# Kernel optimization log

Hardware: AMD Instinct MI355X
Metric: run time of the kernel (lower is better)

The kernel has to match this reference:

```python
import jax, jax.numpy as jnp
import numpy as np
import math

N = 131072        # number of query points
IN_DIM = 3
G = 5             # grid_level = num_sin_layers - 2
F = 8             # feature_dims per level
W = 256           # hidden width (ffenc_dims[1:])
OUT = 64          # num_outputs
BOUND = 1.0
BASE_SIGMA = 1.0
EXP_SIGMA = 2.0
SIN_W0 = 5.0      # multires - 1 = n_levels - 1


def setup_inputs() -> dict:
    key = jax.random.key(0)
    ks = jax.random.split(key, 9)
    in_pos = jax.random.uniform(ks[0], (N, IN_DIM), jnp.float32, -BOUND, BOUND)
    grid_feats = jax.random.normal(ks[1], (N, G * F), jnp.float32) * 0.01  # grid_embed_std
    ffn_A = jax.random.normal(ks[2], (G, F, W), jnp.float32)
    # SIREN-style inits (scaled normals approximating uniform SIREN init ranges)
    W0 = jax.random.normal(ks[3], (IN_DIM, W), jnp.float32) / IN_DIM
    b0 = jax.random.normal(ks[4], (W,), jnp.float32) * 0.01
    Wh = jax.random.normal(ks[5], (G, W, W), jnp.float32) * (math.sqrt(6.0 / W) / SIN_W0)
    bh = jax.random.normal(ks[6], (G, W), jnp.float32) * 0.01
    Wh_high = jax.random.normal(ks[7], (G, W, OUT), jnp.float32) * (math.sqrt(6.0 / W) / SIN_W0)
    bh_high = jax.random.normal(ks[8], (G, OUT), jnp.float32) * 0.01
    return {"in_pos": in_pos, "grid_feats": grid_feats, "ffn_A": ffn_A,
            "W0": W0, "b0": b0, "Wh": Wh, "bh": bh,
            "Wh_high": Wh_high, "bh_high": bh_high}


def reference(in_pos, grid_feats, ffn_A, W0, b0, Wh, bh, Wh_high, bh_high):
    sigmas = BASE_SIGMA * (EXP_SIGMA ** jnp.arange(G, dtype=jnp.float32))  # [G]
    embed = lambda h: jnp.sin(SIN_W0 * h)  # dim-preserving periodic embedding

    x = in_pos / BOUND                                   # [N, 3]
    # grid branch: per-level Fourier projection of hash-grid features
    gx = jnp.transpose(grid_feats.reshape(-1, G, F), (1, 0, 2))  # [G, N, F]
    ffn = ffn_A * sigmas[:, None, None]                   # [G, F, W]
    gx = jnp.sin((2.0 * math.pi) * jnp.einsum('gnf,gfw->gnw', gx, ffn))  # [G, N, W]

    # SIREN branch, layer 0
    x = embed(x @ W0 + b0)                                # [N, W]
    x_out = jnp.zeros((x.shape[0], OUT), dtype=x.dtype)
    for l in range(G):  # layers 1 .. num_sin_layers-2
        x = embed(x @ Wh[l] + bh[l])                      # [N, W]
        x = gx[l] + x                                     # grid residual
        x_out = x_out + embed(x @ Wh_high[l] + bh_high[l])
    return x_out
```

## Files before the change

### kernel.cpp

```cpp
#include <hip/hip_runtime.h>


#define TM 64
#define XSTRIDE 264
#define GSTRIDE 48
#define K5 0.79577471545947667f

typedef __attribute__((ext_vector_type(8))) _Float16 v8h;
typedef __attribute__((ext_vector_type(2))) __fp16 hw2;
typedef __attribute__((ext_vector_type(4))) float v4f;
typedef __attribute__((ext_vector_type(16))) float v16f;

#define MFMA16H(a, b, c) __builtin_amdgcn_mfma_f32_16x16x32_f16(a, b, c, 0, 0, 0)
#define MFMA32H(a, b, c) __builtin_amdgcn_mfma_f32_32x32x16_f16(a, b, c, 0, 0, 0)

__device__ __forceinline__ float sin_rev(float u) {
#if __has_builtin(__builtin_amdgcn_fractf)
    return __builtin_amdgcn_sinf(__builtin_amdgcn_fractf(u));
#else
    return __builtin_amdgcn_sinf(u - floorf(u));
#endif
}

__device__ __forceinline__ short f16s(float x) {
    _Float16 hh = (_Float16)x;
    return __builtin_bit_cast(short, hh);
}

__global__ __launch_bounds__(256) void ffb_pack(
    const float* __restrict__ Wh, const float* __restrict__ Whh,
    const float* __restrict__ ffnA,
    short* __restrict__ wh, short* __restrict__ whh, short* __restrict__ gf)
{
    int t = blockIdx.x * 256 + threadIdx.x;
    if (t < 40960) {
        int lane = t & 63, nt = (t >> 6) & 7, kb = (t >> 9) & 15, l = t >> 13;
        int n = nt * 32 + (lane & 31);
        int k0 = kb * 16 + (lane >> 5) * 8;
        short hs[8];
        #pragma unroll
        for (int jj = 0; jj < 8; jj++)
            hs[jj] = f16s(Wh[(l * 256 + k0 + jj) * 256 + n] * K5);
        *(v8h*)(wh + t * 8) = *(v8h*)hs;
    } else if (t < 51200) {
        int t2 = t - 40960;
        int lane = t2 & 63, nt = (t2 >> 6) & 3, kb = (t2 >> 8) & 7, l = t2 >> 11;
        int n = nt * 16 + (lane & 15);
        int k0 = kb * 32 + (lane >> 4) * 8;
        short hs[8];
        #pragma unroll
        for (int jj = 0; jj < 8; jj++)
            hs[jj] = f16s(Whh[(l * 256 + k0 + jj) * 64 + n] * K5);
        *(v8h*)(whh + t2 * 8) = *(v8h*)hs;
    } else if (t < 53760) {
        int t3 = t - 51200;
        int lane = t3 & 63, nt = (t3 >> 6) & 7, l = t3 >> 9;
        int n = nt * 32 + (lane & 31);
        const float sc = 0.5f * (float)(1 << l);
        short hs[8];
        #pragma unroll
        for (int jj = 0; jj < 8; jj++)
            hs[jj] = f16s(ffnA[(l * 8 + jj) * 256 + n] * sc);
        *(v8h*)(gf + t3 * 8) = *(v8h*)hs;
    }
}

__global__ __launch_bounds__(256, 3) void ffb_main(
    const float* __restrict__ pos, const float* __restrict__ gfeat,
    const float* __restrict__ W0, const float* __restrict__ b0,
    const float* __restrict__ bh, const float* __restrict__ bhh,
    const short* __restrict__ wh, const short* __restrict__ whh,
    const short* __restrict__ gf,
    float* __restrict__ out)
{
    __shared__ __align__(16) short s_x[TM * XSTRIDE];
    __shared__ __align__(16) short s_g[TM * GSTRIDE];
    __shared__ float s_pos[TM * 3];

    const int tid = threadIdx.x;
    const int row0 = blockIdx.x * TM;
    const int lane = tid & 63;
    const int w = tid >> 6;
    const int i = lane & 15;
    const int q = lane >> 4;
    const int m32 = lane & 31;
    const int h = lane >> 5;

    if (tid < TM * 3) s_pos[tid] = pos[row0 * 3 + tid];
    for (int k2 = tid; k2 < TM * 40; k2 += 256) {
        int r = k2 / 40, f = k2 % 40;
        s_g[r * GSTRIDE + f] = f16s(gfeat[row0 * 40 + k2]);
    }
    __syncthreads();

    {
        const int c = tid;
        const float w00 = W0[c], w01 = W0[256 + c], w02 = W0[512 + c], bc = b0[c];
        #pragma unroll 4
        for (int r = 0; r < TM; r++) {
            float d = s_pos[r * 3 + 0] * w00 + s_pos[r * 3 + 1] * w01
                    + s_pos[r * 3 + 2] * w02 + bc;
            s_x[r * XSTRIDE + c] = f16s(sin_rev(d * K5));
        }
    }
    __syncthreads();

    float cout[4][4];
    #pragma unroll
    for (int m = 0; m < 4; m++)
        #pragma unroll
        for (int r = 0; r < 4; r++) cout[m][r] = 0.f;

    const int a1off0 = m32 * XSTRIDE + h * 8;
    const int a1off1 = (32 + m32) * XSTRIDE + h * 8;

    for (int l = 0; l < 5; l++) {
        const float bias0 = bh[l * 256 + w * 64 + m32] * K5;
        const float bias1 = bh[l * 256 + w * 64 + 32 + m32] * K5;
        v16f C1[2][2];
        #pragma unroll
        for (int r = 0; r < 16; r++) {
            C1[0][0][r] = bias0; C1[1][0][r] = bias0;
            C1[0][1][r] = bias1; C1[1][1][r] = bias1;
        }
        v8h gb0 = *(const v8h*)(gf + ((l * 8 + w * 2 + 0) * 64 + lane) * 8);
        v8h gb1 = *(const v8h*)(gf + ((l * 8 + w * 2 + 1) * 64 + lane) * 8);

        {
            const short* bp = wh + l * 65536 + (2 * w) * 512 + lane * 8;
            v8h rb0[4], rb1[4];
            #pragma unroll
            for (int p = 0; p < 3; p++) {
                rb0[p] = *(const v8h*)(bp + p * 4096);
                rb1[p] = *(const v8h*)(bp + p * 4096 + 512);
            }
            #pragma unroll
            for (int kb = 0; kb < 16; kb++) {
                if (kb + 3 < 16) {
                    rb0[(kb + 3) & 3] = *(const v8h*)(bp + (kb + 3) * 4096);
                    rb1[(kb + 3) & 3] = *(const v8h*)(bp + (kb + 3) * 4096 + 512);
                }
                v8h a0 = *(const v8h*)&s_x[a1off0 + kb * 16];
                v8h a1 = *(const v8h*)&s_x[a1off1 + kb * 16];
                v8h bc0 = rb0[kb & 3], bc1 = rb1[kb & 3];
                C1[0][0] = MFMA32H(a0, bc0, C1[0][0]);
                C1[0][1] = MFMA32H(a0, bc1, C1[0][1]);
                C1[1][0] = MFMA32H(a1, bc0, C1[1][0]);
                C1[1][1] = MFMA32H(a1, bc1, C1[1][1]);
            }
        }
        __syncthreads();

        #pragma unroll
        for (int m = 0; m < 2; m++) {
            v8h ga = *(const v8h*)&s_g[(m * 32 + m32) * GSTRIDE + l * 8];
            #pragma unroll
            for (int t = 0; t < 2; t++) {
                v16f Z = {};
                v16f G = MFMA32H(ga, (t ? gb1 : gb0), Z);
                const int col = w * 64 + t * 32 + m32;
                #pragma unroll
                for (int r = 0; r < 16; r++) {
                    const int row = m * 32 + (r & 3) + 8 * (r >> 2) + 4 * h;
                    float v = sin_rev(C1[m][t][r]) + sin_rev(G[r]);
                    s_x[row * XSTRIDE + col] = f16s(v);
                }
            }
        }
        __syncthreads();

        const float b2 = bhh[l * 64 + w * 16 + i] * K5;
        v4f C2[4];
        #pragma unroll
        for (int m = 0; m < 4; m++) C2[m] = (v4f){b2, b2, b2, b2};
        {
            const short* bp = whh + l * 16384 + w * 512 + lane * 8;
            v8h bc[8];
            #pragma unroll
            for (int kb = 0; kb < 8; kb++)
                bc[kb] = *(const v8h*)(bp + kb * 2048);
            #pragma unroll
            for (int kb = 0; kb < 8; kb++) {
                #pragma unroll
                for (int m = 0; m < 4; m++) {
                    v8h a = *(const v8h*)&s_x[(m * 16 + i) * XSTRIDE + q * 8 + kb * 32];
                    C2[m] = MFMA16H(a, bc[kb], C2[m]);
                }
            }
        }
        #pragma unroll
        for (int m = 0; m < 4; m++)
            #pragma unroll
            for (int r = 0; r < 4; r++)
                cout[m][r] += sin_rev(C2[m][r]);
    }

    #pragma unroll
    for (int m = 0; m < 4; m++)
        #pragma unroll
        for (int r = 0; r < 4; r++)
            out[(row0 + m * 16 + q * 4 + r) * 64 + w * 16 + i] = cout[m][r];
}

extern "C" void kernel_launch(void* const* d_in, const int* in_sizes, int n_in,
                              void* d_out, int out_size, void* d_ws, size_t ws_size,
                              hipStream_t stream) {
    const float* pos   = (const float*)d_in[0];
    const float* gfeat = (const float*)d_in[1];
    const float* ffnA  = (const float*)d_in[2];
    const float* W0    = (const float*)d_in[3];
    const float* b0    = (const float*)d_in[4];
    const float* Wh    = (const float*)d_in[5];
    const float* bh    = (const float*)d_in[6];
    const float* Whh   = (const float*)d_in[7];
    const float* bhh   = (const float*)d_in[8];
    float* out = (float*)d_out;
    const int N = in_sizes[0] / 3;

    short* wh  = (short*)d_ws;
    short* whh = wh + 327680;
    short* gf  = whh + 81920;

    ffb_pack<<<210, 256, 0, stream>>>(Wh, Whh, ffnA, wh, whh, gf);
    ffb_main<<<N / TM, 256, 0, stream>>>(pos, gfeat, W0, b0, bh, bhh,
                                         wh, whh, gf, out);
}
```

Before: 229.0 us.

## Transpose MFMA operands for packed LDS stores and use 32x32 tiles for output layer

Swaps the A/B operands of the hidden-layer MFMAs so each lane holds consecutive output columns, which lets the activation write-back to LDS use packed 64-bit stores of four fp16 values instead of scalar 16-bit stores. The output-head GEMM is changed from 16x16x32 tiles (four M tiles per wave) to one 32x32x16 tile per wave, with the packed Whh layout and the output indexing updated to match. Biases are now loaded per-register to fit the transposed accumulator layout. This trims LDS store instructions and bank pressure, at the cost of more scalar bias loads and a different register footprint.

```diff
diff --git a/kernel.cpp b/kernel.cpp
--- a/kernel.cpp
+++ b/kernel.cpp
@@ -7,11 +7,9 @@
 #define K5 0.79577471545947667f
 
 typedef __attribute__((ext_vector_type(8))) _Float16 v8h;
-typedef __attribute__((ext_vector_type(2))) __fp16 hw2;
-typedef __attribute__((ext_vector_type(4))) float v4f;
+typedef __attribute__((ext_vector_type(2))) unsigned int v2u;
 typedef __attribute__((ext_vector_type(16))) float v16f;
 
-#define MFMA16H(a, b, c) __builtin_amdgcn_mfma_f32_16x16x32_f16(a, b, c, 0, 0, 0)
 #define MFMA32H(a, b, c) __builtin_amdgcn_mfma_f32_32x32x16_f16(a, b, c, 0, 0, 0)
 
 __device__ __forceinline__ float sin_rev(float u) {
@@ -22,6 +20,10 @@
 #endif
 }
 
+__device__ __forceinline__ unsigned int f16u(float x) {
+    _Float16 hh = (_Float16)x;
+    return (unsigned int)(unsigned short)__builtin_bit_cast(short, hh);
+}
 __device__ __forceinline__ short f16s(float x) {
     _Float16 hh = (_Float16)x;
     return __builtin_bit_cast(short, hh);
@@ -44,9 +46,9 @@
         *(v8h*)(wh + t * 8) = *(v8h*)hs;
     } else if (t < 51200) {
         int t2 = t - 40960;
-        int lane = t2 & 63, nt = (t2 >> 6) & 3, kb = (t2 >> 8) & 7, l = t2 >> 11;
-        int n = nt * 16 + (lane & 15);
-        int k0 = kb * 32 + (lane >> 4) * 8;
+        int lane = t2 & 63, ct = (t2 >> 6) & 1, kb = (t2 >> 7) & 15, l = t2 >> 11;
+        int n = ct * 32 + (lane & 31);
+        int k0 = kb * 16 + (lane >> 5) * 8;
         short hs[8];
         #pragma unroll
         for (int jj = 0; jj < 8; jj++)
@@ -81,8 +83,6 @@
     const int row0 = blockIdx.x * TM;
     const int lane = tid & 63;
     const int w = tid >> 6;
-    const int i = lane & 15;
-    const int q = lane >> 4;
     const int m32 = lane & 31;
     const int h = lane >> 5;
 
@@ -105,23 +105,25 @@
     }
     __syncthreads();
 
-    float cout[4][4];
+    float cout[16];
     #pragma unroll
-    for (int m = 0; m < 4; m++)
-        #pragma unroll
-        for (int r = 0; r < 4; r++) cout[m][r] = 0.f;
+    for (int r = 0; r < 16; r++) cout[r] = 0.f;
 
     const int a1off0 = m32 * XSTRIDE + h * 8;
     const int a1off1 = (32 + m32) * XSTRIDE + h * 8;
+    const int arowt = ((w & 1) * 32 + m32) * XSTRIDE + h * 8;
+    const int hct = w >> 1;
 
     for (int l = 0; l < 5; l++) {
-        const float bias0 = bh[l * 256 + w * 64 + m32] * K5;
-        const float bias1 = bh[l * 256 + w * 64 + 32 + m32] * K5;
         v16f C1[2][2];
         #pragma unroll
-        for (int r = 0; r < 16; r++) {
-            C1[0][0][r] = bias0; C1[1][0][r] = bias0;
-            C1[0][1][r] = bias1; C1[1][1][r] = bias1;
+        for (int mt = 0; mt < 2; mt++) {
+            const float* bb = bh + l * 256 + w * 64 + mt * 32 + 4 * h;
+            #pragma unroll
+            for (int r = 0; r < 16; r++) {
+                float bv = bb[(r & 3) + 8 * (r >> 2)] * K5;
+                C1[0][mt][r] = bv; C1[1][mt][r] = bv;
+            }
         }
         v8h gb0 = *(const v8h*)(gf + ((l * 8 + w * 2 + 0) * 64 + lane) * 8);
         v8h gb1 = *(const v8h*)(gf + ((l * 8 + w * 2 + 1) * 64 + lane) * 8);
@@ -140,66 +142,68 @@
                     rb0[(kb + 3) & 3] = *(const v8h*)(bp + (kb + 3) * 4096);
                     rb1[(kb + 3) & 3] = *(const v8h*)(bp + (kb + 3) * 4096 + 512);
                 }
-                v8h a0 = *(const v8h*)&s_x[a1off0 + kb * 16];
-                v8h a1 = *(const v8h*)&s_x[a1off1 + kb * 16];
+                v8h x0 = *(const v8h*)&s_x[a1off0 + kb * 16];
+                v8h x1 = *(const v8h*)&s_x[a1off1 + kb * 16];
                 v8h bc0 = rb0[kb & 3], bc1 = rb1[kb & 3];
-                C1[0][0] = MFMA32H(a0, bc0, C1[0][0]);
-                C1[0][1] = MFMA32H(a0, bc1, C1[0][1]);
-                C1[1][0] = MFMA32H(a1, bc0, C1[1][0]);
-                C1[1][1] = MFMA32H(a1, bc1, C1[1][1]);
+                C1[0][0] = MFMA32H(bc0, x0, C1[0][0]);
+                C1[0][1] = MFMA32H(bc1, x0, C1[0][1]);
+                C1[1][0] = MFMA32H(bc0, x1, C1[1][0]);
+                C1[1][1] = MFMA32H(bc1, x1, C1[1][1]);
             }
         }
         __syncthreads();
 
         #pragma unroll
-        for (int m = 0; m < 2; m++) {
-            v8h ga = *(const v8h*)&s_g[(m * 32 + m32) * GSTRIDE + l * 8];
-            #pragma unroll
-            for (int t = 0; t < 2; t++) {
+        for (int nt = 0; nt < 2; nt++) {
+            v8h ga = *(const v8h*)&s_g[(nt * 32 + m32) * GSTRIDE + l * 8];
+            const int rowi = (nt * 32 + m32) * XSTRIDE;
+            #pragma unroll
+            for (int mt = 0; mt < 2; mt++) {
                 v16f Z = {};
-                v16f G = MFMA32H(ga, (t ? gb1 : gb0), Z);
-                const int col = w * 64 + t * 32 + m32;
+                v16f G = MFMA32H((mt ? gb1 : gb0), ga, Z);
+                const int colb = w * 64 + mt * 32 + 4 * h;
                 #pragma unroll
-                for (int r = 0; r < 16; r++) {
-                    const int row = m * 32 + (r & 3) + 8 * (r >> 2) + 4 * h;
-                    float v = sin_rev(C1[m][t][r]) + sin_rev(G[r]);
-                    s_x[row * XSTRIDE + col] = f16s(v);
+                for (int rr = 0; rr < 4; rr++) {
+                    float v0 = sin_rev(C1[nt][mt][rr * 4 + 0]) + sin_rev(G[rr * 4 + 0]);
+                    float v1 = sin_rev(C1[nt][mt][rr * 4 + 1]) + sin_rev(G[rr * 4 + 1]);
+                    float v2 = sin_rev(C1[nt][mt][rr * 4 + 2]) + sin_rev(G[rr * 4 + 2]);
+                    float v3 = sin_rev(C1[nt][mt][rr * 4 + 3]) + sin_rev(G[rr * 4 + 3]);
+                    unsigned int u01 = f16u(v0) | (f16u(v1) << 16);
+                    unsigned int u23 = f16u(v2) | (f16u(v3) << 16);
+                    *(v2u*)&s_x[rowi + colb + 8 * rr] = (v2u){u01, u23};
                 }
             }
         }
         __syncthreads();
 
-        const float b2 = bhh[l * 64 + w * 16 + i] * K5;
-        v4f C2[4];
-        #pragma unroll
-        for (int m = 0; m < 4; m++) C2[m] = (v4f){b2, b2, b2, b2};
+        const float b2 = bhh[l * 64 + hct * 32 + m32] * K5;
+        v16f C2;
+        #pragma unroll
+        for (int r = 0; r < 16; r++) C2[r] = b2;
         {
-            const short* bp = whh + l * 16384 + w * 512 + lane * 8;
-            v8h bc[8];
-            #pragma unroll
-            for (int kb = 0; kb < 8; kb++)
-                bc[kb] = *(const v8h*)(bp + kb * 2048);
-            #pragma unroll
-            for (int kb = 0; kb < 8; kb++) {
-                #pragma unroll
-                for (int m = 0; m < 4; m++) {
-                    v8h a = *(const v8h*)&s_x[(m * 16 + i) * XSTRIDE + q * 8 + kb * 32];
-                    C2[m] = MFMA16H(a, bc[kb], C2[m]);
-                }
-            }
-        }
-        #pragma unroll
-        for (int m = 0; m < 4; m++)
-            #pragma unroll
-            for (int r = 0; r < 4; r++)
-                cout[m][r] += sin_rev(C2[m][r]);
+            const short* bp = whh + l * 16384 + hct * 512 + lane * 8;
+            v8h rb[4];
+            #pragma unroll
+            for (int p = 0; p < 3; p++)
+                rb[p] = *(const v8h*)(bp + p * 1024);
+            #pragma unroll
+            for (int kb = 0; kb < 16; kb++) {
+                if (kb + 3 < 16)
+                    rb[(kb + 3) & 3] = *(const v8h*)(bp + (kb + 3) * 1024);
+                v8h a = *(const v8h*)&s_x[arowt + kb * 16];
+                C2 = MFMA32H(a, rb[kb & 3], C2);
+            }
+        }
+        #pragma unroll
+        for (int r = 0; r < 16; r++)
+            cout[r] += sin_rev(C2[r]);
     }
 
     #pragma unroll
-    for (int m = 0; m < 4; m++)
-        #pragma unroll
-        for (int r = 0; r < 4; r++)
-            out[(row0 + m * 16 + q * 4 + r) * 64 + w * 16 + i] = cout[m][r];
+    for (int r = 0; r < 16; r++) {
+        const int row = (w & 1) * 32 + (r & 3) + 8 * (r >> 2) + 4 * h;
+        out[(row0 + row) * 64 + hct * 32 + m32] = cout[r];
+    }
 }
 
 extern "C" void kernel_launch(void* const* d_in, const int* in_sizes, int n_in,
```

New measurement: 239.0 us. +4.4%, slower.
